# Optimization experiments

Hardware: AMD Instinct MI355X
Metric: run time of the kernel (lower is better)

The kernel has to match this reference:

```python
import jax, jax.numpy as jnp
import numpy as np

W_WORDS = 30  # hardcoded by `temp[i][30*j+k]` in the original module


def setup_inputs() -> dict:
    key = jax.random.key(0)
    k1, k2 = jax.random.split(key)
    input_var = jax.random.randint(k1, (32, 32, W_WORDS), 0, 50000, dtype=jnp.int64)
    W_emb = jax.random.normal(k2, (50000, 300), dtype=jnp.float32)
    return {"input_var": input_var, "W_emb": W_emb}


def reference(input_var, W_emb):
    B, S, W = input_var.shape
    E = W_emb.shape[1]

    mask3 = input_var != 0                               # [B,S,W]
    word_mask = mask3.reshape(-1, W).astype(jnp.uint8)   # [B*S, W]
    sent_mask = (mask3.sum(axis=2) != 0).astype(jnp.uint8)  # [B,S]

    # Vectorized version of the triple loop: keep tokens up to the FIRST zero
    # in each sentence (the loop `break`s on the first zero), zero the rest.
    keep = jnp.cumprod(mask3.astype(jnp.int32), axis=2).astype(bool)  # [B,S,W]
    temp = jnp.where(keep, input_var, 0).reshape(B, S * W)            # [B, S*W]
    mask = (temp != 0).astype(jnp.uint8)                              # [B, S*W]

    # model_type == 'word' branch; dropout p=0 is identity
    embedded = W_emb[input_var].reshape(-1, W, E)   # [B*S, W, E]
    share_enc_embedded = W_emb[temp]                # [B, S*W, E]

    return embedded, share_enc_embedded, mask, word_mask, sent_mask
```

## Files before the change

### kernel.cpp

```cpp
#include <hip/hip_runtime.h>

constexpr int B  = 32;
constexpr int S  = 32;
constexpr int W  = 30;
constexpr int E  = 300;
constexpr int EV = E / 4;
constexpr int NSENT = B * S;

constexpr long OFF_EMB   = 0;
constexpr long OFF_SHARE = (long)NSENT * W * E;
constexpr long OFF_MASK  = OFF_SHARE + (long)NSENT * W * E;
constexpr long OFF_WM    = OFF_MASK + (long)NSENT * W;
constexpr long OFF_SM    = OFF_WM + (long)NSENT * W;

__global__ __launch_bounds__(256) void embed_gather_kernel(
    const int* __restrict__ input,
    const float* __restrict__ Wemb,
    float* __restrict__ out)
{
    const int sent = blockIdx.x;
    const int tid  = threadIdx.x;

    __shared__ int idx_s[W];
    __shared__ int tidx_s[W];
    __shared__ int zpos_s;

    if (tid < W) idx_s[tid] = input[sent * W + tid];
    __syncthreads();

    if (tid == 0) {
        int z = W;
        int any = 0;
        for (int k = 0; k < W; ++k) {
            int v = idx_s[k];
            any |= (v != 0);
            if (v == 0 && z == W) z = k;
        }
        zpos_s = z;
        out[OFF_SM + sent] = any ? 1.0f : 0.0f;
    }
    __syncthreads();

    const int z = zpos_s;
    if (tid < W) {
        int idx = idx_s[tid];
        int tix = (tid < z) ? idx : 0;
        tidx_s[tid] = tix;
        out[OFF_WM   + (long)sent * W + tid] = (idx != 0) ? 1.0f : 0.0f;
        out[OFF_MASK + (long)sent * W + tid] = (tix != 0) ? 1.0f : 0.0f;
    }
    __syncthreads();

    const float4* __restrict__ W4 = (const float4*)Wemb;
    float4* __restrict__ oe = (float4*)(out + OFF_EMB);
    float4* __restrict__ os = (float4*)(out + OFF_SHARE);
    const long sbase = (long)sent * W * EV;

    for (int i = tid; i < W * EV; i += 256) {
        int k = i / EV;
        int q = i - k * EV;
        int idx = idx_s[k];
        int tix = tidx_s[k];
        float4 a = W4[(long)idx * EV + q];
        float4 b = (tix == idx) ? a : W4[(long)tix * EV + q];
        oe[sbase + i] = a;
        os[sbase + i] = b;
    }
}

extern "C" void kernel_launch(void* const* d_in, const int* in_sizes, int n_in,
                              void* d_out, int out_size, void* d_ws, size_t ws_size,
                              hipStream_t stream) {
    const int*   input = (const int*)d_in[0];
    const float* Wemb  = (const float*)d_in[1];
    float*       out   = (float*)d_out;

    embed_gather_kernel<<<NSENT, 256, 0, stream>>>(input, Wemb, out);
}
```

Before: 120.6 us.

## Split mask prep into separate kernel and flatten gather to one float4 per thread

Moves the per-sentence zero-position and mask computation into a small prep kernel that writes zpos to workspace. The gather becomes a flat grid with one float4 per thread, with no shared memory and no block barriers, so the 1024-block launch with idle threads during the serial scan is gone. This costs an extra kernel launch and an extra per-thread read of the index and zpos. It also loses the per-block reuse of indices and runs the prep kernel on only 4 blocks with strided per-thread writes.

```diff
diff --git a/kernel.cpp b/kernel.cpp
--- a/kernel.cpp
+++ b/kernel.cpp
@@ -6,66 +6,67 @@
 constexpr int E  = 300;
 constexpr int EV = E / 4;
 constexpr int NSENT = B * S;
+constexpr int NTOK  = NSENT * W;
+constexpr int NF4   = NTOK * EV;
 
 constexpr long OFF_EMB   = 0;
-constexpr long OFF_SHARE = (long)NSENT * W * E;
-constexpr long OFF_MASK  = OFF_SHARE + (long)NSENT * W * E;
-constexpr long OFF_WM    = OFF_MASK + (long)NSENT * W;
-constexpr long OFF_SM    = OFF_WM + (long)NSENT * W;
+constexpr long OFF_SHARE = (long)NTOK * E;
+constexpr long OFF_MASK  = OFF_SHARE + (long)NTOK * E;
+constexpr long OFF_WM    = OFF_MASK + (long)NTOK;
+constexpr long OFF_SM    = OFF_WM + (long)NTOK;
 
-__global__ __launch_bounds__(256) void embed_gather_kernel(
+__global__ __launch_bounds__(256) void prep_kernel(
     const int* __restrict__ input,
+    float* __restrict__ out,
+    int* __restrict__ zarr)
+{
+    const int sent = blockIdx.x * 256 + threadIdx.x;
+    if (sent >= NSENT) return;
+
+    int vals[W];
+    #pragma unroll
+    for (int k = 0; k < W; ++k) vals[k] = input[sent * W + k];
+
+    int z = W, any = 0;
+    #pragma unroll
+    for (int k = 0; k < W; ++k) {
+        any |= (vals[k] != 0);
+        if (vals[k] == 0 && z == W) z = k;
+    }
+
+    zarr[sent] = z;
+    out[OFF_SM + sent] = any ? 1.0f : 0.0f;
+
+    #pragma unroll
+    for (int k = 0; k < W; ++k) {
+        out[OFF_WM   + (long)sent * W + k] = (vals[k] != 0) ? 1.0f : 0.0f;
+        out[OFF_MASK + (long)sent * W + k] = (k < z) ? 1.0f : 0.0f;
+    }
+}
+
+__global__ __launch_bounds__(256) void gather_kernel(
+    const int* __restrict__ input,
+    const int* __restrict__ zarr,
     const float* __restrict__ Wemb,
     float* __restrict__ out)
 {
-    const int sent = blockIdx.x;
-    const int tid  = threadIdx.x;
+    const int g = blockIdx.x * 256 + threadIdx.x;
 
-    __shared__ int idx_s[W];
-    __shared__ int tidx_s[W];
-    __shared__ int zpos_s;
+    const int token = g / EV;
+    const int q     = g - token * EV;
+    const int sent  = token / W;
+    const int k     = token - sent * W;
 
-    if (tid < W) idx_s[tid] = input[sent * W + tid];
-    __syncthreads();
-
-    if (tid == 0) {
-        int z = W;
-        int any = 0;
-        for (int k = 0; k < W; ++k) {
-            int v = idx_s[k];
-            any |= (v != 0);
-            if (v == 0 && z == W) z = k;
-        }
-        zpos_s = z;
-        out[OFF_SM + sent] = any ? 1.0f : 0.0f;
-    }
-    __syncthreads();
-
-    const int z = zpos_s;
-    if (tid < W) {
-        int idx = idx_s[tid];
-        int tix = (tid < z) ? idx : 0;
-        tidx_s[tid] = tix;
-        out[OFF_WM   + (long)sent * W + tid] = (idx != 0) ? 1.0f : 0.0f;
-        out[OFF_MASK + (long)sent * W + tid] = (tix != 0) ? 1.0f : 0.0f;
-    }
-    __syncthreads();
+    const int idx = input[token];
+    const int z   = zarr[sent];
+    const int tix = (k < z) ? idx : 0;
 
     const float4* __restrict__ W4 = (const float4*)Wemb;
-    float4* __restrict__ oe = (float4*)(out + OFF_EMB);
-    float4* __restrict__ os = (float4*)(out + OFF_SHARE);
-    const long sbase = (long)sent * W * EV;
+    float4 a = W4[(long)idx * EV + q];
+    float4 b = (tix == idx) ? a : W4[(long)q];
 
-    for (int i = tid; i < W * EV; i += 256) {
-        int k = i / EV;
-        int q = i - k * EV;
-        int idx = idx_s[k];
-        int tix = tidx_s[k];
-        float4 a = W4[(long)idx * EV + q];
-        float4 b = (tix == idx) ? a : W4[(long)tix * EV + q];
-        oe[sbase + i] = a;
-        os[sbase + i] = b;
-    }
+    ((float4*)(out + OFF_EMB))[g]   = a;
+    ((float4*)(out + OFF_SHARE))[g] = b;
 }
 
 extern "C" void kernel_launch(void* const* d_in, const int* in_sizes, int n_in,
@@ -74,6 +75,8 @@
     const int*   input = (const int*)d_in[0];
     const float* Wemb  = (const float*)d_in[1];
     float*       out   = (float*)d_out;
+    int*         zarr  = (int*)d_ws;
 
-    embed_gather_kernel<<<NSENT, 256, 0, stream>>>(input, Wemb, out);
+    prep_kernel<<<(NSENT + 255) / 256, 256, 0, stream>>>(input, out, zarr);
+    gather_kernel<<<NF4 / 256, 256, 0, stream>>>(input, zarr, Wemb, out);
 }
```

New measurement: 121.6 us. Within noise of the previous version (+0.8%).
